# Kernel optimization log

Hardware: AMD Instinct MI355X
Metric: run time of the kernel (lower is better)

Reference implementation:

```python
import jax, jax.numpy as jnp
import numpy as np

BN_EPS = 1e-5

def setup_inputs() -> dict:
    key = jax.random.key(0)
    ks = jax.random.split(key, 8)
    C = 64
    NB, N_SP = 256, 64          # num blocks, spatial n (size3d = (1, 64, 64))
    N = NB * N_SP * N_SP        # 1,048,576 total rows
    s = np.sqrt(2.0 / C).astype(np.float32)   # kaiming_normal fan_in scale
    s2 = np.sqrt(2.0 / (2 * C)).astype(np.float32)
    return {
        "x":   jax.random.normal(ks[0], (N, C), jnp.float32),
        "w11": jax.random.normal(ks[1], (C, C), jnp.float32) * s,
        "b11": jnp.zeros((C,), jnp.float32),
        "w12": jax.random.normal(ks[2], (C, C), jnp.float32) * s,
        "b12": jnp.zeros((C,), jnp.float32),
        "w21": jax.random.normal(ks[3], (C, C), jnp.float32) * s,
        "b21": jnp.zeros((C,), jnp.float32),
        "w22": jax.random.normal(ks[4], (C, C), jnp.float32) * s,
        "b22": jnp.zeros((C,), jnp.float32),
        "uW1": jax.random.normal(ks[5], (2 * C, C), jnp.float32) * s2,
        "ub1": jnp.zeros((C,), jnp.float32),
        "g1":  jnp.ones((C,), jnp.float32),
        "be1": jnp.zeros((C,), jnp.float32),
        "uW2": jax.random.normal(ks[6], (C, C), jnp.float32) * s,
        "ub2": jnp.zeros((C,), jnp.float32),
        "g2":  jnp.ones((C,), jnp.float32),
        "be2": jnp.zeros((C,), jnp.float32),
        "num_blocks": NB,
        "blk_n": N_SP,
    }

def _block_mlp(h, params):
    # 1x1 Conv2d stack == per-position channel matmul; W is (out_ch, in_ch)
    for W, b in params:
        h = jax.nn.relu(jnp.einsum('bijc,oc->bijo', h, W) + b)
    return h

def _bn_relu(z, g, b):
    # BatchNorm1d, training mode: batch mean / biased batch var
    mu = jnp.mean(z, axis=0)
    var = jnp.var(z, axis=0)
    return jax.nn.relu((z - mu) * jax.lax.rsqrt(var + BN_EPS) * g + b)

def reference(x, w11, b11, w12, b12, w21, b21, w22, b22,
              uW1, ub1, g1, be1, uW2, ub2, g2, be2, num_blocks, blk_n):
    C = x.shape[-1]
    # uniform blocks: split + reshape to (b=1, n, n, C) -> fold into one array
    xb = x.reshape(num_blocks, blk_n, blk_n, C)          # NHWC (block, i, j, c)
    m1 = _block_mlp(xb, [(w11, b11), (w12, b12)])
    m2 = _block_mlp(xb, [(w21, b21), (w22, b22)])
    # torch.matmul over trailing spatial dims, batched over (block, channel)
    corr = jnp.einsum('bikc,bkjc->bijc', m1, m2)
    h = jnp.sqrt(jax.nn.relu(corr)).reshape(-1, C)
    h = jnp.concatenate([x, h], axis=1)                  # [N, 2C]
    h = _bn_relu(h @ uW1 + ub1, g1, be1)
    h = _bn_relu(h @ uW2 + ub2, g2, be2)
    return h + x
```

## Files before the change

kernel.cpp:

```cpp
#include <hip/hip_runtime.h>

#define NROWS   1048576
#define SBLK    4096

using bfrag = __attribute__((ext_vector_type(8))) short;
using ffrag = __attribute__((ext_vector_type(4))) float;

__device__ __forceinline__ float bf2f(unsigned short u) {
    unsigned w = ((unsigned)u) << 16;
    return __builtin_bit_cast(float, w);
}
__device__ __forceinline__ unsigned short f2bf(float f) {
    unsigned u = __builtin_bit_cast(unsigned, f);
    u += 0x7fffu + ((u >> 16) & 1u);
    return (unsigned short)(u >> 16);
}
__device__ __forceinline__ short pk(float f) { return (short)f2bf(f); }

__global__ void k_prep(const float* __restrict__ w11, const float* __restrict__ w12,
                       const float* __restrict__ w21, const float* __restrict__ w22,
                       const float* __restrict__ uW1, const float* __restrict__ uW2,
                       unsigned short* __restrict__ w11b, unsigned short* __restrict__ w12b,
                       unsigned short* __restrict__ w21b, unsigned short* __restrict__ w22b,
                       unsigned short* __restrict__ uW1bt, unsigned short* __restrict__ uW2bt)
{
    int t = threadIdx.x;
    for (int i = t; i < 4096; i += 256) {
        w11b[i] = f2bf(w11[i]);
        w12b[i] = f2bf(w12[i]);
        w21b[i] = f2bf(w21[i]);
        w22b[i] = f2bf(w22[i]);
        int o = i >> 6, c = i & 63;
        uW2bt[o * 64 + c] = f2bf(uW2[c * 64 + o]);
    }
    for (int i = t; i < 8192; i += 256) {
        int o = i >> 7, c = i & 127;
        uW1bt[o * 128 + c] = f2bf(uW1[c * 64 + o]);
    }
}

__global__ __launch_bounds__(256) void k_mlp(
    const float* __restrict__ x,
    const unsigned short* __restrict__ w11b, const float* __restrict__ b11,
    const unsigned short* __restrict__ w12b, const float* __restrict__ b12,
    const unsigned short* __restrict__ w21b, const float* __restrict__ b21,
    const unsigned short* __restrict__ w22b, const float* __restrict__ b22,
    unsigned short* __restrict__ M1, unsigned short* __restrict__ M2)
{
    __shared__ unsigned short xs[64 * 72];
    __shared__ unsigned short ts[64 * 72];
    __shared__ unsigned short t2[64 * 67];
    const int t   = threadIdx.x;
    const int w   = t >> 6, ln = t & 63;
    const int col = ln & 15, q = ln >> 4;

    for (int blk = blockIdx.x; blk < NROWS / 64; blk += gridDim.x) {
        const int n0 = blk * 64;
        const int b = n0 >> 12, s0 = n0 & (SBLK - 1);

        const float4* X4 = reinterpret_cast<const float4*>(x) + (size_t)n0 * 16;
        #pragma unroll
        for (int j = 0; j < 4; ++j) {
            int i = t + j * 256;
            float4 v = X4[i];
            int row = i >> 4, c0 = (i & 15) * 4;
            unsigned lo = ((unsigned)f2bf(v.x)) | ((unsigned)f2bf(v.y) << 16);
            unsigned hi = ((unsigned)f2bf(v.z)) | ((unsigned)f2bf(v.w) << 16);
            *reinterpret_cast<uint2*>(&xs[row * 72 + c0]) = make_uint2(lo, hi);
        }
        __syncthreads();

        #pragma unroll
        for (int br = 0; br < 2; ++br) {
            const unsigned short* wA = br ? w21b : w11b;
            const unsigned short* wB = br ? w22b : w12b;
            const float* bA = br ? b21 : b11;
            const float* bB = br ? b22 : b12;
            unsigned short* M = br ? M2 : M1;

            bfrag bw[2][4];
            #pragma unroll
            for (int kt = 0; kt < 2; ++kt)
                #pragma unroll
                for (int ct = 0; ct < 4; ++ct)
                    bw[kt][ct] = *reinterpret_cast<const bfrag*>(
                        wA + (ct * 16 + col) * 64 + kt * 32 + q * 8);
            bfrag a0 = *reinterpret_cast<const bfrag*>(&xs[(w * 16 + col) * 72 + q * 8]);
            bfrag a1 = *reinterpret_cast<const bfrag*>(&xs[(w * 16 + col) * 72 + 32 + q * 8]);
            #pragma unroll
            for (int ct = 0; ct < 4; ++ct) {
                ffrag acc = {0.f, 0.f, 0.f, 0.f};
                acc = __builtin_amdgcn_mfma_f32_16x16x32_bf16(a0, bw[0][ct], acc, 0, 0, 0);
                acc = __builtin_amdgcn_mfma_f32_16x16x32_bf16(a1, bw[1][ct], acc, 0, 0, 0);
                float bias = bA[ct * 16 + col];
                #pragma unroll
                for (int r = 0; r < 4; ++r) {
                    float v = fmaxf(acc[r] + bias, 0.f);
                    ts[(w * 16 + q * 4 + r) * 72 + ct * 16 + col] = f2bf(v);
                }
            }
            #pragma unroll
            for (int kt = 0; kt < 2; ++kt)
                #pragma unroll
                for (int ct = 0; ct < 4; ++ct)
                    bw[kt][ct] = *reinterpret_cast<const bfrag*>(
                        wB + (ct * 16 + col) * 64 + kt * 32 + q * 8);
            a0 = *reinterpret_cast<const bfrag*>(&ts[(w * 16 + col) * 72 + q * 8]);
            a1 = *reinterpret_cast<const bfrag*>(&ts[(w * 16 + col) * 72 + 32 + q * 8]);
            #pragma unroll
            for (int ct = 0; ct < 4; ++ct) {
                ffrag acc = {0.f, 0.f, 0.f, 0.f};
                acc = __builtin_amdgcn_mfma_f32_16x16x32_bf16(a0, bw[0][ct], acc, 0, 0, 0);
                acc = __builtin_amdgcn_mfma_f32_16x16x32_bf16(a1, bw[1][ct], acc, 0, 0, 0);
                float bias = bB[ct * 16 + col];
                #pragma unroll
                for (int r = 0; r < 4; ++r) {
                    float v = fmaxf(acc[r] + bias, 0.f);
                    t2[(w * 16 + q * 4 + r) * 67 + ct * 16 + col] = f2bf(v);
                }
            }
            __syncthreads();
            unsigned short* Mp = M + ((size_t)b << 18) + s0 + ln;
            #pragma unroll
            for (int i = 0; i < 16; ++i) {
                int o = w * 16 + i;
                Mp[(size_t)o * SBLK] = t2[ln * 67 + o];
            }
            __syncthreads();
        }
    }
}

__global__ __launch_bounds__(256) void k_corr(
    unsigned short* __restrict__ M1, const unsigned short* __restrict__ M2)
{
    __shared__ float As[64 * 68];
    __shared__ float Bs[64 * 68];
    const int t = threadIdx.x;
    const size_t base = (size_t)blockIdx.x << 12;
    const uint4* A4 = reinterpret_cast<const uint4*>(M1 + base);
    const uint4* B4 = reinterpret_cast<const uint4*>(M2 + base);

    #pragma unroll
    for (int l = 0; l < 2; ++l) {
        int f8 = t + l * 256;
        uint4 pa = A4[f8];
        uint4 pb = B4[f8];
        int f = f8 * 8;
        int row = f >> 6;
        int col0 = f & 63;
        unsigned pav[4] = { pa.x, pa.y, pa.z, pa.w };
        unsigned pbv[4] = { pb.x, pb.y, pb.z, pb.w };
        #pragma unroll
        for (int m = 0; m < 4; ++m) {
            As[(col0 + 2 * m + 0) * 68 + row] = bf2f((unsigned short)(pav[m] & 0xffff));
            As[(col0 + 2 * m + 1) * 68 + row] = bf2f((unsigned short)(pav[m] >> 16));
            Bs[row * 68 + col0 + 2 * m + 0]   = bf2f((unsigned short)(pbv[m] & 0xffff));
            Bs[row * 68 + col0 + 2 * m + 1]   = bf2f((unsigned short)(pbv[m] >> 16));
        }
    }
    __syncthreads();

    const int tj = t & 15, ti = t >> 4;
    float acc[4][4];
    #pragma unroll
    for (int r = 0; r < 4; ++r)
        #pragma unroll
        for (int c = 0; c < 4; ++c) acc[r][c] = 0.f;

    for (int k = 0; k < 64; ++k) {
        float4 a  = *reinterpret_cast<const float4*>(&As[k * 68 + 4 * ti]);
        float4 bv = *reinterpret_cast<const float4*>(&Bs[k * 68 + 4 * tj]);
        float av[4] = { a.x, a.y, a.z, a.w };
        float bb[4] = { bv.x, bv.y, bv.z, bv.w };
        #pragma unroll
        for (int r = 0; r < 4; ++r)
            #pragma unroll
            for (int c = 0; c < 4; ++c)
                acc[r][c] = fmaf(av[r], bb[c], acc[r][c]);
    }

    unsigned short* Hp = M1 + base;
    #pragma unroll
    for (int r = 0; r < 4; ++r) {
        ushort4 hv;
        hv.x = f2bf(sqrtf(fmaxf(acc[r][0], 0.f)));
        hv.y = f2bf(sqrtf(fmaxf(acc[r][1], 0.f)));
        hv.z = f2bf(sqrtf(fmaxf(acc[r][2], 0.f)));
        hv.w = f2bf(sqrtf(fmaxf(acc[r][3], 0.f)));
        *reinterpret_cast<ushort4*>(&Hp[(4 * ti + r) * 64 + 4 * tj]) = hv;
    }
}

__global__ __launch_bounds__(256) void k_fc1(
    const float* __restrict__ x, const unsigned short* __restrict__ H,
    const unsigned short* __restrict__ uW1bt, const float* __restrict__ ub1,
    unsigned short* __restrict__ Z1, float* __restrict__ sum1, float* __restrict__ sq1)
{
    __shared__ unsigned short hs[64 * 72];
    __shared__ float redS[4][64], redQ[4][64];
    const int t   = threadIdx.x;
    const int w   = t >> 6, ln = t & 63;
    const int col = ln & 15, q = ln >> 4;

    bfrag bw[4][4];
    #pragma unroll
    for (int kt = 0; kt < 4; ++kt)
        #pragma unroll
        for (int ct = 0; ct < 4; ++ct)
            bw[kt][ct] = *reinterpret_cast<const bfrag*>(
                uW1bt + (ct * 16 + col) * 128 + kt * 32 + q * 8);
    float bias[4];
    #pragma unroll
    for (int ct = 0; ct < 4; ++ct) bias[ct] = ub1[ct * 16 + col];

    float sA[4] = {0, 0, 0, 0}, qA[4] = {0, 0, 0, 0};

    for (int blk = blockIdx.x; blk < NROWS / 64; blk += gridDim.x) {
        const int n0 = blk * 64;
        const int b = n0 >> 12, s0 = n0 & (SBLK - 1);

        {
            const int c = t & 63, ch = t >> 6;
            const unsigned short* hp = H + ((size_t)b << 18) + (size_t)c * SBLK + s0 + ch * 16;
            uint4 p0 = reinterpret_cast<const uint4*>(hp)[0];
            uint4 p1 = reinterpret_cast<const uint4*>(hp)[1];
            unsigned pv[8] = { p0.x, p0.y, p0.z, p0.w, p1.x, p1.y, p1.z, p1.w };
            #pragma unroll
            for (int m = 0; m < 8; ++m) {
                int s = ch * 16 + m * 2;
                hs[(s + 0) * 72 + c] = (unsigned short)(pv[m] & 0xffff);
                hs[(s + 1) * 72 + c] = (unsigned short)(pv[m] >> 16);
            }
        }
        __syncthreads();

        const int row = w * 16 + col;
        bfrag ax[2];
        #pragma unroll
        for (int kt = 0; kt < 2; ++kt) {
            const float* xp = x + (size_t)(n0 + row) * 64 + kt * 32 + q * 8;
            float4 lo = reinterpret_cast<const float4*>(xp)[0];
            float4 hi = reinterpret_cast<const float4*>(xp)[1];
            bfrag a;
            a[0] = pk(lo.x); a[1] = pk(lo.y); a[2] = pk(lo.z); a[3] = pk(lo.w);
            a[4] = pk(hi.x); a[5] = pk(hi.y); a[6] = pk(hi.z); a[7] = pk(hi.w);
            ax[kt] = a;
        }
        bfrag ah0 = *reinterpret_cast<const bfrag*>(&hs[row * 72 + q * 8]);
        bfrag ah1 = *reinterpret_cast<const bfrag*>(&hs[row * 72 + 32 + q * 8]);

        #pragma unroll
        for (int ct = 0; ct < 4; ++ct) {
            ffrag acc = {0.f, 0.f, 0.f, 0.f};
            acc = __builtin_amdgcn_mfma_f32_16x16x32_bf16(ax[0], bw[0][ct], acc, 0, 0, 0);
            acc = __builtin_amdgcn_mfma_f32_16x16x32_bf16(ax[1], bw[1][ct], acc, 0, 0, 0);
            acc = __builtin_amdgcn_mfma_f32_16x16x32_bf16(ah0,  bw[2][ct], acc, 0, 0, 0);
            acc = __builtin_amdgcn_mfma_f32_16x16x32_bf16(ah1,  bw[3][ct], acc, 0, 0, 0);
            #pragma unroll
            for (int r = 0; r < 4; ++r) {
                float v = acc[r] + bias[ct];
                Z1[(size_t)(n0 + w * 16 + q * 4 + r) * 64 + ct * 16 + col] = f2bf(v);
                sA[ct] += v; qA[ct] += v * v;
            }
        }
        __syncthreads();
    }

    #pragma unroll
    for (int ct = 0; ct < 4; ++ct) {
        float s = sA[ct], qq = qA[ct];
        s  += __shfl_xor(s, 16);  s  += __shfl_xor(s, 32);
        qq += __shfl_xor(qq, 16); qq += __shfl_xor(qq, 32);
        if (q == 0) { redS[w][ct * 16 + col] = s; redQ[w][ct * 16 + col] = qq; }
    }
    __syncthreads();
    if (t < 64) {
        float S = redS[0][t] + redS[1][t] + redS[2][t] + redS[3][t];
        float Q = redQ[0][t] + redQ[1][t] + redQ[2][t] + redQ[3][t];
        atomicAdd(&sum1[t], S);
        atomicAdd(&sq1[t], Q);
    }
}

__global__ void k_final(const float* __restrict__ sum, const float* __restrict__ sq,
                        const float* __restrict__ g, const float* __restrict__ be,
                        float* __restrict__ scale, float* __restrict__ shift)
{
    int c = threadIdx.x;
    if (c < 64) {
        const float invN = 1.f / (float)NROWS;
        float mu  = sum[c] * invN;
        float var = sq[c] * invN - mu * mu;
        float rs  = rsqrtf(var + 1e-5f);
        float sc  = g[c] * rs;
        scale[c] = sc;
        shift[c] = be[c] - mu * sc;
    }
}

__global__ __launch_bounds__(256) void k_fc2(
    const unsigned short* __restrict__ Z1, const unsigned short* __restrict__ uW2bt,
    const float* __restrict__ ub2, const float* __restrict__ scale1,
    const float* __restrict__ shift1,
    unsigned short* __restrict__ Z2, float* __restrict__ sum2, float* __restrict__ sq2)
{
    __shared__ float redS[4][64], redQ[4][64];
    const int t   = threadIdx.x;
    const int w   = t >> 6, ln = t & 63;
    const int col = ln & 15, q = ln >> 4;

    bfrag bw[2][4];
    #pragma unroll
    for (int kt = 0; kt < 2; ++kt)
        #pragma unroll
        for (int ct = 0; ct < 4; ++ct)
            bw[kt][ct] = *reinterpret_cast<const bfrag*>(
                uW2bt + (ct * 16 + col) * 64 + kt * 32 + q * 8);
    float bias[4];
    #pragma unroll
    for (int ct = 0; ct < 4; ++ct) bias[ct] = ub2[ct * 16 + col];
    float sc[2][8], sh[2][8];
    #pragma unroll
    for (int kt = 0; kt < 2; ++kt)
        #pragma unroll
        for (int j = 0; j < 8; ++j) {
            int c = kt * 32 + q * 8 + j;
            sc[kt][j] = scale1[c];
            sh[kt][j] = shift1[c];
        }

    float sA[4] = {0, 0, 0, 0}, qA[4] = {0, 0, 0, 0};

    const int wg = blockIdx.x * 4 + w;
    const int stride = gridDim.x * 4;
    for (int tile = wg; tile < NROWS / 16; tile += stride) {
        const size_t rbase = (size_t)tile * 16;
        bfrag a[2];
        #pragma unroll
        for (int kt = 0; kt < 2; ++kt) {
            const unsigned short* zp = Z1 + (rbase + col) * 64 + kt * 32 + q * 8;
            uint4 p = *reinterpret_cast<const uint4*>(zp);
            unsigned pv[4] = { p.x, p.y, p.z, p.w };
            bfrag av;
            #pragma unroll
            for (int m = 0; m < 4; ++m) {
                float lo = bf2f((unsigned short)(pv[m] & 0xffff));
                float hi = bf2f((unsigned short)(pv[m] >> 16));
                lo = fmaxf(fmaf(lo, sc[kt][2 * m],     sh[kt][2 * m]),     0.f);
                hi = fmaxf(fmaf(hi, sc[kt][2 * m + 1], sh[kt][2 * m + 1]), 0.f);
                av[2 * m] = pk(lo); av[2 * m + 1] = pk(hi);
            }
            a[kt] = av;
        }
        #pragma unroll
        for (int ct = 0; ct < 4; ++ct) {
            ffrag acc = {0.f, 0.f, 0.f, 0.f};
            acc = __builtin_amdgcn_mfma_f32_16x16x32_bf16(a[0], bw[0][ct], acc, 0, 0, 0);
            acc = __builtin_amdgcn_mfma_f32_16x16x32_bf16(a[1], bw[1][ct], acc, 0, 0, 0);
            #pragma unroll
            for (int r = 0; r < 4; ++r) {
                float v = acc[r] + bias[ct];
                Z2[(rbase + q * 4 + r) * 64 + ct * 16 + col] = f2bf(v);
                sA[ct] += v; qA[ct] += v * v;
            }
        }
    }

    #pragma unroll
    for (int ct = 0; ct < 4; ++ct) {
        float s = sA[ct], qq = qA[ct];
        s  += __shfl_xor(s, 16);  s  += __shfl_xor(s, 32);
        qq += __shfl_xor(qq, 16); qq += __shfl_xor(qq, 32);
        if (q == 0) { redS[w][ct * 16 + col] = s; redQ[w][ct * 16 + col] = qq; }
    }
    __syncthreads();
    if (t < 64) {
        float S = redS[0][t] + redS[1][t] + redS[2][t] + redS[3][t];
        float Q = redQ[0][t] + redQ[1][t] + redQ[2][t] + redQ[3][t];
        atomicAdd(&sum2[t], S);
        atomicAdd(&sq2[t], Q);
    }
}

__global__ __launch_bounds__(256) void k_out(
    const float* __restrict__ x, const unsigned short* __restrict__ Z2,
    const float* __restrict__ scale2, const float* __restrict__ shift2,
    float* __restrict__ out)
{
    const int i  = blockIdx.x * 256 + threadIdx.x;
    const int c0 = (i & 15) * 4;
    float4 xv = reinterpret_cast<const float4*>(x)[i];
    ushort4 zv = reinterpret_cast<const ushort4*>(Z2)[i];
    float4 o;
    o.x = fmaxf(fmaf(bf2f(zv.x), scale2[c0 + 0], shift2[c0 + 0]), 0.f) + xv.x;
    o.y = fmaxf(fmaf(bf2f(zv.y), scale2[c0 + 1], shift2[c0 + 1]), 0.f) + xv.y;
    o.z = fmaxf(fmaf(bf2f(zv.z), scale2[c0 + 2], shift2[c0 + 2]), 0.f) + xv.z;
    o.w = fmaxf(fmaf(bf2f(zv.w), scale2[c0 + 3], shift2[c0 + 3]), 0.f) + xv.w;
    reinterpret_cast<float4*>(out)[i] = o;
}

extern "C" void kernel_launch(void* const* d_in, const int* in_sizes, int n_in,
                              void* d_out, int out_size, void* d_ws, size_t ws_size,
                              hipStream_t stream)
{
    const float* x   = (const float*)d_in[0];
    const float* w11 = (const float*)d_in[1];
    const float* b11 = (const float*)d_in[2];
    const float* w12 = (const float*)d_in[3];
    const float* b12 = (const float*)d_in[4];
    const float* w21 = (const float*)d_in[5];
    const float* b21 = (const float*)d_in[6];
    const float* w22 = (const float*)d_in[7];
    const float* b22 = (const float*)d_in[8];
    const float* uW1 = (const float*)d_in[9];
    const float* ub1 = (const float*)d_in[10];
    const float* g1  = (const float*)d_in[11];
    const float* be1 = (const float*)d_in[12];
    const float* uW2 = (const float*)d_in[13];
    const float* ub2 = (const float*)d_in[14];
    const float* g2  = (const float*)d_in[15];
    const float* be2 = (const float*)d_in[16];

    char* ws = (char*)d_ws;
    const size_t BUF = (size_t)NROWS * 64 * sizeof(unsigned short);
    unsigned short* B0 = (unsigned short*)ws;
    unsigned short* B1 = (unsigned short*)(ws + BUF);
    float* stats  = (float*)(ws + 2 * BUF);
    float* sum1   = stats;        float* sq1    = stats + 64;
    float* sum2   = stats + 128;  float* sq2    = stats + 192;
    float* scale1 = stats + 256;  float* shift1 = stats + 320;
    float* scale2 = stats + 384;  float* shift2 = stats + 448;
    unsigned short* wb = (unsigned short*)(ws + 2 * BUF + 2048);
    unsigned short* w11b  = wb;
    unsigned short* w12b  = wb + 4096;
    unsigned short* w21b  = wb + 8192;
    unsigned short* w22b  = wb + 12288;
    unsigned short* uW1bt = wb + 16384;
    unsigned short* uW2bt = wb + 24576;

    hipMemsetAsync(stats, 0, 256 * sizeof(float), stream);

    k_prep<<<1, 256, 0, stream>>>(w11, w12, w21, w22, uW1, uW2,
                                  w11b, w12b, w21b, w22b, uW1bt, uW2bt);
    k_mlp<<<2048, 256, 0, stream>>>(x, w11b, b11, w12b, b12, w21b, b21, w22b, b22, B0, B1);
    k_corr<<<16384, 256, 0, stream>>>(B0, B1);
    k_fc1<<<2048, 256, 0, stream>>>(x, B0, uW1bt, ub1, B1, sum1, sq1);
    k_final<<<1, 64, 0, stream>>>(sum1, sq1, g1, be1, scale1, shift1);
    k_fc2<<<2048, 256, 0, stream>>>(B1, uW2bt, ub2, scale1, shift1, B0, sum2, sq2);
    k_final<<<1, 64, 0, stream>>>(sum2, sq2, g2, be2, scale2, shift2);
    k_out<<<NROWS * 64 / 4 / 256, 256, 0, stream>>>(x, B0, scale2, shift2, (float*)d_out);
}
```

Before: 1.022 ms.

## Rework MLP, corr and fc1 kernels around per-wave tiles and MFMA correlation

```diff
diff --git a/kernel.cpp b/kernel.cpp
--- a/kernel.cpp
+++ b/kernel.cpp
@@ -5,6 +5,7 @@
 
 using bfrag = __attribute__((ext_vector_type(8))) short;
 using ffrag = __attribute__((ext_vector_type(4))) float;
+using uifrag = __attribute__((ext_vector_type(4))) unsigned;
 
 __device__ __forceinline__ float bf2f(unsigned short u) {
     unsigned w = ((unsigned)u) << 16;
@@ -16,6 +17,11 @@
     return (unsigned short)(u >> 16);
 }
 __device__ __forceinline__ short pk(float f) { return (short)f2bf(f); }
+__device__ __forceinline__ unsigned cvtpk(float lo, float hi) {
+    unsigned r;
+    asm("v_cvt_pk_bf16_f32 %0, %1, %2" : "=v"(r) : "v"(lo), "v"(hi));
+    return r;
+}
 
 __global__ void k_prep(const float* __restrict__ w11, const float* __restrict__ w12,
                        const float* __restrict__ w21, const float* __restrict__ w22,
@@ -39,7 +45,7 @@
     }
 }
 
-__global__ __launch_bounds__(256) void k_mlp(
+__global__ __launch_bounds__(256, 3) void k_mlp(
     const float* __restrict__ x,
     const unsigned short* __restrict__ w11b, const float* __restrict__ b11,
     const unsigned short* __restrict__ w12b, const float* __restrict__ b12,
@@ -47,28 +53,33 @@
     const unsigned short* __restrict__ w22b, const float* __restrict__ b22,
     unsigned short* __restrict__ M1, unsigned short* __restrict__ M2)
 {
-    __shared__ unsigned short xs[64 * 72];
-    __shared__ unsigned short ts[64 * 72];
-    __shared__ unsigned short t2[64 * 67];
+    __shared__ unsigned short ts[4][64 * 72];
     const int t   = threadIdx.x;
     const int w   = t >> 6, ln = t & 63;
     const int col = ln & 15, q = ln >> 4;
-
-    for (int blk = blockIdx.x; blk < NROWS / 64; blk += gridDim.x) {
-        const int n0 = blk * 64;
+    unsigned short* tsw = ts[w];
+
+    const int nw = gridDim.x * 4;
+    for (int tile = blockIdx.x * 4 + w; tile < NROWS / 64; tile += nw) {
+        const int n0 = tile * 64;
         const int b = n0 >> 12, s0 = n0 & (SBLK - 1);
 
-        const float4* X4 = reinterpret_cast<const float4*>(x) + (size_t)n0 * 16;
-        #pragma unroll
-        for (int j = 0; j < 4; ++j) {
-            int i = t + j * 256;
-            float4 v = X4[i];
-            int row = i >> 4, c0 = (i & 15) * 4;
-            unsigned lo = ((unsigned)f2bf(v.x)) | ((unsigned)f2bf(v.y) << 16);
-            unsigned hi = ((unsigned)f2bf(v.z)) | ((unsigned)f2bf(v.w) << 16);
-            *reinterpret_cast<uint2*>(&xs[row * 72 + c0]) = make_uint2(lo, hi);
-        }
-        __syncthreads();
+        bfrag ax[4][2];
+        #pragma unroll
+        for (int mt = 0; mt < 4; ++mt) {
+            const float* xr = x + (size_t)(n0 + mt * 16 + col) * 64 + q * 8;
+            #pragma unroll
+            for (int kt = 0; kt < 2; ++kt) {
+                float4 lo = *reinterpret_cast<const float4*>(xr + kt * 32);
+                float4 hi = *reinterpret_cast<const float4*>(xr + kt * 32 + 4);
+                uifrag u;
+                u[0] = cvtpk(lo.x, lo.y);
+                u[1] = cvtpk(lo.z, lo.w);
+                u[2] = cvtpk(hi.x, hi.y);
+                u[3] = cvtpk(hi.z, hi.w);
+                ax[mt][kt] = __builtin_bit_cast(bfrag, u);
+            }
+        }
 
         #pragma unroll
         for (int br = 0; br < 2; ++br) {
@@ -76,119 +87,107 @@
             const unsigned short* wB = br ? w22b : w12b;
             const float* bA = br ? b21 : b11;
             const float* bB = br ? b22 : b12;
-            unsigned short* M = br ? M2 : M1;
-
-            bfrag bw[2][4];
-            #pragma unroll
-            for (int kt = 0; kt < 2; ++kt)
+            unsigned short* Mb = (br ? M2 : M1) + ((size_t)b << 18) + s0;
+
+            bfrag  bw[4][2];
+            float4 bsv[4];
+            #pragma unroll
+            for (int ot = 0; ot < 4; ++ot) {
                 #pragma unroll
-                for (int ct = 0; ct < 4; ++ct)
-                    bw[kt][ct] = *reinterpret_cast<const bfrag*>(
-                        wA + (ct * 16 + col) * 64 + kt * 32 + q * 8);
-            bfrag a0 = *reinterpret_cast<const bfrag*>(&xs[(w * 16 + col) * 72 + q * 8]);
-            bfrag a1 = *reinterpret_cast<const bfrag*>(&xs[(w * 16 + col) * 72 + 32 + q * 8]);
-            #pragma unroll
-            for (int ct = 0; ct < 4; ++ct) {
-                ffrag acc = {0.f, 0.f, 0.f, 0.f};
-                acc = __builtin_amdgcn_mfma_f32_16x16x32_bf16(a0, bw[0][ct], acc, 0, 0, 0);
-                acc = __builtin_amdgcn_mfma_f32_16x16x32_bf16(a1, bw[1][ct], acc, 0, 0, 0);
-                float bias = bA[ct * 16 + col];
+                for (int kt = 0; kt < 2; ++kt)
+                    bw[ot][kt] = *reinterpret_cast<const bfrag*>(
+                        wA + (ot * 16 + col) * 64 + kt * 32 + q * 8);
+                bsv[ot] = *reinterpret_cast<const float4*>(bA + ot * 16 + q * 4);
+            }
+            #pragma unroll
+            for (int mt = 0; mt < 4; ++mt) {
                 #pragma unroll
-                for (int r = 0; r < 4; ++r) {
-                    float v = fmaxf(acc[r] + bias, 0.f);
-                    ts[(w * 16 + q * 4 + r) * 72 + ct * 16 + col] = f2bf(v);
+                for (int ot = 0; ot < 4; ++ot) {
+                    ffrag acc = {0.f, 0.f, 0.f, 0.f};
+                    acc = __builtin_amdgcn_mfma_f32_16x16x32_bf16(bw[ot][0], ax[mt][0], acc, 0, 0, 0);
+                    acc = __builtin_amdgcn_mfma_f32_16x16x32_bf16(bw[ot][1], ax[mt][1], acc, 0, 0, 0);
+                    float4 bs = bsv[ot];
+                    unsigned u0 = cvtpk(fmaxf(acc[0] + bs.x, 0.f), fmaxf(acc[1] + bs.y, 0.f));
+                    unsigned u1 = cvtpk(fmaxf(acc[2] + bs.z, 0.f), fmaxf(acc[3] + bs.w, 0.f));
+                    *reinterpret_cast<uint2*>(&tsw[(mt * 16 + col) * 72 + ot * 16 + q * 4]) =
+                        make_uint2(u0, u1);
                 }
             }
             #pragma unroll
-            for (int kt = 0; kt < 2; ++kt)
+            for (int ot = 0; ot < 4; ++ot) {
                 #pragma unroll
-                for (int ct = 0; ct < 4; ++ct)
-                    bw[kt][ct] = *reinterpret_cast<const bfrag*>(
-                        wB + (ct * 16 + col) * 64 + kt * 32 + q * 8);
-            a0 = *reinterpret_cast<const bfrag*>(&ts[(w * 16 + col) * 72 + q * 8]);
-            a1 = *reinterpret_cast<const bfrag*>(&ts[(w * 16 + col) * 72 + 32 + q * 8]);
-            #pragma unroll
-            for (int ct = 0; ct < 4; ++ct) {
-                ffrag acc = {0.f, 0.f, 0.f, 0.f};
-                acc = __builtin_amdgcn_mfma_f32_16x16x32_bf16(a0, bw[0][ct], acc, 0, 0, 0);
-                acc = __builtin_amdgcn_mfma_f32_16x16x32_bf16(a1, bw[1][ct], acc, 0, 0, 0);
-                float bias = bB[ct * 16 + col];
+                for (int kt = 0; kt < 2; ++kt)
+                    bw[ot][kt] = *reinterpret_cast<const bfrag*>(
+                        wB + (ot * 16 + col) * 64 + kt * 32 + q * 8);
+                bsv[ot] = *reinterpret_cast<const float4*>(bB + ot * 16 + q * 4);
+            }
+            #pragma unroll
+            for (int mt = 0; mt < 4; ++mt) {
+                bfrag az0 = *reinterpret_cast<const bfrag*>(&tsw[(mt * 16 + col) * 72 + q * 8]);
+                bfrag az1 = *reinterpret_cast<const bfrag*>(&tsw[(mt * 16 + col) * 72 + 32 + q * 8]);
                 #pragma unroll
-                for (int r = 0; r < 4; ++r) {
-                    float v = fmaxf(acc[r] + bias, 0.f);
-                    t2[(w * 16 + q * 4 + r) * 67 + ct * 16 + col] = f2bf(v);
+                for (int ot = 0; ot < 4; ++ot) {
+                    ffrag acc = {0.f, 0.f, 0.f, 0.f};
+                    acc = __builtin_amdgcn_mfma_f32_16x16x32_bf16(bw[ot][0], az0, acc, 0, 0, 0);
+                    acc = __builtin_amdgcn_mfma_f32_16x16x32_bf16(bw[ot][1], az1, acc, 0, 0, 0);
+                    float4 bs = bsv[ot];
+                    unsigned u0 = cvtpk(fmaxf(acc[0] + bs.x, 0.f), fmaxf(acc[1] + bs.y, 0.f));
+                    unsigned u1 = cvtpk(fmaxf(acc[2] + bs.z, 0.f), fmaxf(acc[3] + bs.w, 0.f));
+                    unsigned short* mp = Mb + (size_t)(ot * 16 + q * 4) * SBLK + mt * 16 + col;
+                    mp[0]        = (unsigned short)u0;
+                    mp[SBLK]     = (unsigned short)(u0 >> 16);
+                    mp[2 * SBLK] = (unsigned short)u1;
+                    mp[3 * SBLK] = (unsigned short)(u1 >> 16);
                 }
             }
-            __syncthreads();
-            unsigned short* Mp = M + ((size_t)b << 18) + s0 + ln;
-            #pragma unroll
-            for (int i = 0; i < 16; ++i) {
-                int o = w * 16 + i;
-                Mp[(size_t)o * SBLK] = t2[ln * 67 + o];
-            }
-            __syncthreads();
-        }
-    }
-}
-
-__global__ __launch_bounds__(256) void k_corr(
+        }
+    }
+}
+
+__global__ __launch_bounds__(256, 4) void k_corr(
     unsigned short* __restrict__ M1, const unsigned short* __restrict__ M2)
 {
-    __shared__ float As[64 * 68];
-    __shared__ float Bs[64 * 68];
-    const int t = threadIdx.x;
-    const size_t base = (size_t)blockIdx.x << 12;
-    const uint4* A4 = reinterpret_cast<const uint4*>(M1 + base);
-    const uint4* B4 = reinterpret_cast<const uint4*>(M2 + base);
-
-    #pragma unroll
-    for (int l = 0; l < 2; ++l) {
-        int f8 = t + l * 256;
-        uint4 pa = A4[f8];
-        uint4 pb = B4[f8];
-        int f = f8 * 8;
-        int row = f >> 6;
-        int col0 = f & 63;
-        unsigned pav[4] = { pa.x, pa.y, pa.z, pa.w };
-        unsigned pbv[4] = { pb.x, pb.y, pb.z, pb.w };
-        #pragma unroll
-        for (int m = 0; m < 4; ++m) {
-            As[(col0 + 2 * m + 0) * 68 + row] = bf2f((unsigned short)(pav[m] & 0xffff));
-            As[(col0 + 2 * m + 1) * 68 + row] = bf2f((unsigned short)(pav[m] >> 16));
-            Bs[row * 68 + col0 + 2 * m + 0]   = bf2f((unsigned short)(pbv[m] & 0xffff));
-            Bs[row * 68 + col0 + 2 * m + 1]   = bf2f((unsigned short)(pbv[m] >> 16));
+    __shared__ unsigned short Bt[4][64 * 72];
+    const int t   = threadIdx.x;
+    const int w   = t >> 6, ln = t & 63;
+    const int col = ln & 15, q = ln >> 4;
+    const size_t cb = (size_t)blockIdx.x << 14;
+
+    const int k = t >> 2, j0 = (t & 3) * 16;
+    #pragma unroll
+    for (int cc = 0; cc < 4; ++cc) {
+        const unsigned short* Bc = M2 + cb + cc * 4096 + (size_t)k * 64 + j0;
+        uint4 p0 = reinterpret_cast<const uint4*>(Bc)[0];
+        uint4 p1 = reinterpret_cast<const uint4*>(Bc)[1];
+        unsigned pv[8] = { p0.x, p0.y, p0.z, p0.w, p1.x, p1.y, p1.z, p1.w };
+        #pragma unroll
+        for (int m = 0; m < 8; ++m) {
+            Bt[cc][(j0 + 2 * m) * 72 + k]     = (unsigned short)(pv[m] & 0xffff);
+            Bt[cc][(j0 + 2 * m + 1) * 72 + k] = (unsigned short)(pv[m] >> 16);
         }
     }
     __syncthreads();
 
-    const int tj = t & 15, ti = t >> 4;
-    float acc[4][4];
-    #pragma unroll
-    for (int r = 0; r < 4; ++r)
-        #pragma unroll
-        for (int c = 0; c < 4; ++c) acc[r][c] = 0.f;
-
-    for (int k = 0; k < 64; ++k) {
-        float4 a  = *reinterpret_cast<const float4*>(&As[k * 68 + 4 * ti]);
-        float4 bv = *reinterpret_cast<const float4*>(&Bs[k * 68 + 4 * tj]);
-        float av[4] = { a.x, a.y, a.z, a.w };
-        float bb[4] = { bv.x, bv.y, bv.z, bv.w };
-        #pragma unroll
-        for (int r = 0; r < 4; ++r)
-            #pragma unroll
-            for (int c = 0; c < 4; ++c)
-                acc[r][c] = fmaf(av[r], bb[c], acc[r][c]);
-    }
-
-    unsigned short* Hp = M1 + base;
-    #pragma unroll
-    for (int r = 0; r < 4; ++r) {
-        ushort4 hv;
-        hv.x = f2bf(sqrtf(fmaxf(acc[r][0], 0.f)));
-        hv.y = f2bf(sqrtf(fmaxf(acc[r][1], 0.f)));
-        hv.z = f2bf(sqrtf(fmaxf(acc[r][2], 0.f)));
-        hv.w = f2bf(sqrtf(fmaxf(acc[r][3], 0.f)));
-        *reinterpret_cast<ushort4*>(&Hp[(4 * ti + r) * 64 + 4 * tj]) = hv;
+    #pragma unroll
+    for (int cc = 0; cc < 4; ++cc) {
+        unsigned short* Ac = M1 + cb + cc * 4096;
+        bfrag a0 = *reinterpret_cast<const bfrag*>(Ac + (w * 16 + col) * 64 + q * 8);
+        bfrag a1 = *reinterpret_cast<const bfrag*>(Ac + (w * 16 + col) * 64 + 32 + q * 8);
+        #pragma unroll
+        for (int nj = 0; nj < 4; ++nj) {
+            bfrag bq0 = *reinterpret_cast<const bfrag*>(&Bt[cc][(nj * 16 + col) * 72 + q * 8]);
+            bfrag bq1 = *reinterpret_cast<const bfrag*>(&Bt[cc][(nj * 16 + col) * 72 + 32 + q * 8]);
+            ffrag acc = {0.f, 0.f, 0.f, 0.f};
+            acc = __builtin_amdgcn_mfma_f32_16x16x32_bf16(a0, bq0, acc, 0, 0, 0);
+            acc = __builtin_amdgcn_mfma_f32_16x16x32_bf16(a1, bq1, acc, 0, 0, 0);
+            unsigned u0 = cvtpk(sqrtf(fmaxf(acc[0], 0.f)), sqrtf(fmaxf(acc[1], 0.f)));
+            unsigned u1 = cvtpk(sqrtf(fmaxf(acc[2], 0.f)), sqrtf(fmaxf(acc[3], 0.f)));
+            unsigned short* hp = Ac + (size_t)(w * 16 + q * 4) * 64 + nj * 16 + col;
+            hp[0]   = (unsigned short)u0;
+            hp[64]  = (unsigned short)(u0 >> 16);
+            hp[128] = (unsigned short)u1;
+            hp[192] = (unsigned short)(u1 >> 16);
+        }
     }
 }
 
@@ -197,11 +196,12 @@
     const unsigned short* __restrict__ uW1bt, const float* __restrict__ ub1,
     unsigned short* __restrict__ Z1, float* __restrict__ sum1, float* __restrict__ sq1)
 {
-    __shared__ unsigned short hs[64 * 72];
+    __shared__ unsigned short hs[4][16 * 72];
     __shared__ float redS[4][64], redQ[4][64];
     const int t   = threadIdx.x;
     const int w   = t >> 6, ln = t & 63;
     const int col = ln & 15, q = ln >> 4;
+    unsigned short* hsw = hs[w];
 
     bfrag bw[4][4];
     #pragma unroll
@@ -221,19 +221,16 @@
         const int b = n0 >> 12, s0 = n0 & (SBLK - 1);
 
         {
-            const int c = t & 63, ch = t >> 6;
-            const unsigned short* hp = H + ((size_t)b << 18) + (size_t)c * SBLK + s0 + ch * 16;
+            const unsigned short* hp = H + ((size_t)b << 18) + (size_t)ln * SBLK + s0 + w * 16;
             uint4 p0 = reinterpret_cast<const uint4*>(hp)[0];
             uint4 p1 = reinterpret_cast<const uint4*>(hp)[1];
             unsigned pv[8] = { p0.x, p0.y, p0.z, p0.w, p1.x, p1.y, p1.z, p1.w };
             #pragma unroll
             for (int m = 0; m < 8; ++m) {
-                int s = ch * 16 + m * 2;
-                hs[(s + 0) * 72 + c] = (unsigned short)(pv[m] & 0xffff);
-                hs[(s + 1) * 72 + c] = (unsigned short)(pv[m] >> 16);
-            }
-        }
-        __syncthreads();
+                hsw[(2 * m + 0) * 72 + ln] = (unsigned short)(pv[m] & 0xffff);
+                hsw[(2 * m + 1) * 72 + ln] = (unsigned short)(pv[m] >> 16);
+            }
+        }
 
         const int row = w * 16 + col;
         bfrag ax[2];
@@ -242,13 +239,15 @@
             const float* xp = x + (size_t)(n0 + row) * 64 + kt * 32 + q * 8;
             float4 lo = reinterpret_cast<const float4*>(xp)[0];
             float4 hi = reinterpret_cast<const float4*>(xp)[1];
-            bfrag a;
-            a[0] = pk(lo.x); a[1] = pk(lo.y); a[2] = pk(lo.z); a[3] = pk(lo.w);
-            a[4] = pk(hi.x); a[5] = pk(hi.y); a[6] = pk(hi.z); a[7] = pk(hi.w);
-            ax[kt] = a;
-        }
-        bfrag ah0 = *reinterpret_cast<const bfrag*>(&hs[row * 72 + q * 8]);
-        bfrag ah1 = *reinterpret_cast<const bfrag*>(&hs[row * 72 + 32 + q * 8]);
+            uifrag u;
+            u[0] = cvtpk(lo.x, lo.y);
+            u[1] = cvtpk(lo.z, lo.w);
+            u[2] = cvtpk(hi.x, hi.y);
+            u[3] = cvtpk(hi.z, hi.w);
+            ax[kt] = __builtin_bit_cast(bfrag, u);
+        }
+        bfrag ah0 = *reinterpret_cast<const bfrag*>(&hsw[col * 72 + q * 8]);
+        bfrag ah1 = *reinterpret_cast<const bfrag*>(&hsw[col * 72 + 32 + q * 8]);
 
         #pragma unroll
         for (int ct = 0; ct < 4; ++ct) {
@@ -264,7 +263,6 @@
                 sA[ct] += v; qA[ct] += v * v;
             }
         }
-        __syncthreads();
     }
 
     #pragma unroll
@@ -444,7 +442,7 @@
     k_prep<<<1, 256, 0, stream>>>(w11, w12, w21, w22, uW1, uW2,
                                   w11b, w12b, w21b, w22b, uW1bt, uW2bt);
     k_mlp<<<2048, 256, 0, stream>>>(x, w11b, b11, w12b, b12, w21b, b21, w22b, b22, B0, B1);
-    k_corr<<<16384, 256, 0, stream>>>(B0, B1);
+    k_corr<<<4096, 256, 0, stream>>>(B0, B1);
     k_fc1<<<2048, 256, 0, stream>>>(x, B0, uW1bt, ub1, B1, sum1, sq1);
     k_final<<<1, 64, 0, stream>>>(sum1, sq1, g1, be1, scale1, shift1);
     k_fc2<<<2048, 256, 0, stream>>>(B1, uW2bt, ub2, scale1, shift1, B0, sum2, sq2);
```

Measured after the change: 998.4 us. -2.3%, faster.
